# Performance work log

Hardware: AMD Instinct MI355X
Metric: run time of the kernel (lower is better)

Reference implementation:

```python
import jax, jax.numpy as jnp
import numpy as np


def setup_inputs() -> dict:
    key = jax.random.key(0)
    ks = jax.random.split(key, 9)
    bs, nf, h, w = 4, 512, 64, 64
    c8 = nf // 8
    sc = 1.0 / np.sqrt(nf)
    return {
        "x": jax.random.normal(ks[0], (bs, nf, h, w), dtype=jnp.float32),
        "Wq": jax.random.normal(ks[1], (c8, nf), dtype=jnp.float32) * sc,
        "bq": jax.random.normal(ks[2], (c8,), dtype=jnp.float32) * 0.01,
        "Wk": jax.random.normal(ks[3], (c8, nf), dtype=jnp.float32) * sc,
        "bk": jax.random.normal(ks[4], (c8,), dtype=jnp.float32) * 0.01,
        "Wv": jax.random.normal(ks[5], (nf, nf), dtype=jnp.float32) * sc,
        "bv": jax.random.normal(ks[6], (nf,), dtype=jnp.float32) * 0.01,
        "alpha": jax.random.normal(ks[7], (1,), dtype=jnp.float32) * 0.1,
    }


def reference(x, Wq, bq, Wk, bk, Wv, bv, alpha):
    bs, nf, h, w = x.shape
    hw = h * w
    xf = x.reshape(bs, nf, hw)  # flatten spatial; 1x1 conv == channel matmul
    q = jnp.einsum('oc,bcn->bon', Wq, xf) + bq[:, None]  # (bs, c8, hw)
    k = jnp.einsum('oc,bcn->bon', Wk, xf) + bk[:, None]  # (bs, c8, hw)
    v = jnp.einsum('oc,bcn->bon', Wv, xf) + bv[:, None]  # (bs, nf, hw)
    # scores[b, i, j] = key_i . query_j ; softmax over j (queries)
    scores = jnp.einsum('bci,bcj->bij', k, q)  # (bs, hw, hw)
    attn = jax.nn.softmax(scores, axis=-1)
    # out[b, c, i] = sum_j v[b, c, j] * attn[b, i, j]
    out = jnp.einsum('bcj,bij->bci', v, attn).reshape(bs, nf, h, w)
    return x + alpha * out
```

## Files before the change

kernel.cpp:

```cpp
#include <hip/hip_runtime.h>

#define BS 4
#define NF 512
#define HW 4096
#define C8 64
#define TI 32

typedef unsigned short bfu;
typedef __attribute__((ext_vector_type(8))) short bf16x8;
typedef __attribute__((ext_vector_type(4))) float f32x4;

static __device__ __forceinline__ bfu f2bu(float v) {
    union { unsigned int u; float f; } c; c.f = v;
    unsigned int u = c.u;
    u = u + 0x7FFFu + ((u >> 16) & 1u);
    return (bfu)(u >> 16);
}

static __device__ __forceinline__ void gload16(const void* g, void* l) {
    __builtin_amdgcn_global_load_lds(
        (const __attribute__((address_space(1))) unsigned int*)g,
        (__attribute__((address_space(3))) unsigned int*)l,
        16, 0, 0);
}

__global__ __launch_bounds__(256) void k0_xt(const float* __restrict__ x, bfu* __restrict__ xt)
{
    __shared__ float T[64][68];
    const int t  = threadIdx.x;
    const int n0 = blockIdx.x * 64;
    const int c0 = blockIdx.y * 64;
    const int b  = blockIdx.z;

    #pragma unroll
    for (int u = 0; u < 4; u++) {
        int f4 = u * 256 + t;
        int cc = f4 >> 4;
        int n4 = (f4 & 15) << 2;
        float4 v = *(const float4*)(x + ((size_t)(b * NF + c0 + cc)) * HW + n0 + n4);
        *(float4*)&T[cc][n4] = v;
    }
    __syncthreads();
    #pragma unroll
    for (int u = 0; u < 2; u++) {
        int e8 = u * 256 + t;
        int nn = e8 >> 3;
        int c8 = (e8 & 7) << 3;
        union { int4 i4; bfu h[8]; } pk;
        #pragma unroll
        for (int q = 0; q < 8; q++) pk.h[q] = f2bu(T[c8 + q][nn]);
        *(int4*)(xt + ((size_t)(b * HW + n0 + nn)) * NF + c0 + c8) = pk.i4;
    }
}

__global__ __launch_bounds__(256) void k0_w(const float* __restrict__ Wq, const float* __restrict__ bq,
                                            const float* __restrict__ Wk, const float* __restrict__ bk,
                                            const float* __restrict__ Wv, const float* __restrict__ bv,
                                            bfu* __restrict__ Wb, float* __restrict__ bcat)
{
    const int o = blockIdx.x;
    const int t = threadIdx.x;
    const float* src; float bias;
    if (o < 64)       { src = Wq + (size_t)o * NF;          bias = bq[o]; }
    else if (o < 128) { src = Wk + (size_t)(o - 64) * NF;   bias = bk[o - 64]; }
    else              { src = Wv + (size_t)(o - 128) * NF;  bias = bv[o - 128]; }
    float2 v = *(const float2*)(src + t * 2);
    Wb[(size_t)o * NF + t * 2 + 0] = f2bu(v.x);
    Wb[(size_t)o * NF + t * 2 + 1] = f2bu(v.y);
    if (t == 0) bcat[o] = bias;
}

__global__ __launch_bounds__(256) void k1_proj(const bfu* __restrict__ Wb, const float* __restrict__ bcat,
                                               const bfu* __restrict__ xt,
                                               bfu* __restrict__ Qb, bfu* __restrict__ Kb, bfu* __restrict__ Vb)
{
    __shared__ bfu As[128 * 64];
    __shared__ bfu Bs[128 * 64];
    const int t  = threadIdx.x;
    const int o0 = blockIdx.x * 128;
    const int n0 = blockIdx.y * 128;
    const int b  = blockIdx.z;
    const int lane = t & 63, wv = t >> 6;
    const int wm = wv & 1, wn = wv >> 1;
    const int l15 = lane & 15, quad = lane >> 4;

    const int srow = t >> 3;
    const int scol = (t & 7) * 8;

    const bfu* gA = Wb + ((size_t)(o0 + srow)) * NF + scol;
    const bfu* gB = xt + ((size_t)(b * HW + n0 + srow)) * NF + scol;
    bfu* lA = As + t * 8;
    bfu* lB = Bs + t * 8;

    f32x4 acc[4][4];
    #pragma unroll
    for (int m = 0; m < 4; m++)
        #pragma unroll
        for (int n = 0; n < 4; n++) acc[m][n] = (f32x4){0.f, 0.f, 0.f, 0.f};

    for (int c0 = 0; c0 < NF; c0 += 64) {
        __syncthreads();
        #pragma unroll
        for (int p = 0; p < 4; p++) {
            gload16(gA + (size_t)(p * 32) * NF + c0, lA + p * 2048);
            gload16(gB + (size_t)(p * 32) * NF + c0, lB + p * 2048);
        }
        __syncthreads();

        #pragma unroll
        for (int kk = 0; kk < 64; kk += 32) {
            bf16x8 Af[4], Bf[4];
            #pragma unroll
            for (int m = 0; m < 4; m++)
                Af[m] = *(const bf16x8*)(As + (wm * 64 + m * 16 + l15) * 64 + kk + quad * 8);
            #pragma unroll
            for (int n = 0; n < 4; n++)
                Bf[n] = *(const bf16x8*)(Bs + (wn * 64 + n * 16 + l15) * 64 + kk + quad * 8);
            #pragma unroll
            for (int m = 0; m < 4; m++)
                #pragma unroll
                for (int n = 0; n < 4; n++)
                    acc[m][n] = __builtin_amdgcn_mfma_f32_16x16x32_bf16(Af[m], Bf[n], acc[m][n], 0, 0, 0);
        }
    }

    #pragma unroll
    for (int mt = 0; mt < 4; mt++)
        #pragma unroll
        for (int nt = 0; nt < 4; nt++)
            #pragma unroll
            for (int r = 0; r < 4; r++) {
                int go = o0 + wm * 64 + mt * 16 + quad * 4 + r;
                int n  = n0 + wn * 64 + nt * 16 + l15;
                float val = acc[mt][nt][r] + bcat[go];
                if (go < 64)
                    Qb[((size_t)(b * HW + n)) * C8 + go] = f2bu(val);
                else if (go < 128)
                    Kb[((size_t)(b * HW + n)) * C8 + (go - 64)] = f2bu(val);
                else
                    Vb[((size_t)(b * NF + (go - 128))) * HW + n] = f2bu(val);
            }
}

__global__ __launch_bounds__(512, 4) void k23_fused(const bfu* __restrict__ Kb, const bfu* __restrict__ Qb,
                                                    const bfu* __restrict__ Vb,
                                                    const float* __restrict__ x, const float* __restrict__ alpha,
                                                    float* __restrict__ out)
{
    __shared__ bfu   Vs[512 * 64];
    __shared__ bfu   Ps[TI * 72];
    __shared__ float LSum[8][16];
    __shared__ float Scale[TI];

    const int t = threadIdx.x;
    const int lane = t & 63, w = t >> 6;
    const int l15 = lane & 15, quad = lane >> 4;
    const int iq = w >> 2, jq = w & 3;
    const int cw = w * 64;
    const int i0 = blockIdx.x * TI;
    const int b  = blockIdx.y;

    const bfu* kp = Kb + ((size_t)(b * HW + i0 + iq * 16 + l15)) * C8 + quad * 8;
    const bf16x8 Kf0 = *(const bf16x8*)kp;
    const bf16x8 Kf1 = *(const bf16x8*)(kp + 32);

    const bfu* gV = Vb + ((size_t)(b * NF + (t >> 3))) * HW + (t & 7) * 8;
    bfu* lV = Vs + t * 8;

    const bfu* qbase = Qb + ((size_t)(b * HW + jq * 16 + l15)) * C8 + quad * 8;

    f32x4 acc[4][2];
    #pragma unroll
    for (int mt = 0; mt < 4; mt++)
        #pragma unroll
        for (int nt = 0; nt < 2; nt++) acc[mt][nt] = (f32x4){0.f, 0.f, 0.f, 0.f};
    float rsum = 0.f;

    for (int q = 0; q < HW / 64; q++) {
        const int jb = q * 64;
        #pragma unroll
        for (int p = 0; p < 8; p++)
            gload16(gV + (size_t)(p * 64) * HW + jb, lV + p * 4096);

        const bfu* qp = qbase + (size_t)jb * C8;
        bf16x8 A0 = *(const bf16x8*)qp;
        bf16x8 A1 = *(const bf16x8*)(qp + 32);
        f32x4 s = (f32x4){0.f, 0.f, 0.f, 0.f};
        s = __builtin_amdgcn_mfma_f32_16x16x32_bf16(A0, Kf0, s, 0, 0, 0);
        s = __builtin_amdgcn_mfma_f32_16x16x32_bf16(A1, Kf1, s, 0, 0, 0);
        float e0 = __expf(s[0]);
        float e1 = __expf(s[1]);
        float e2 = __expf(s[2]);
        float e3 = __expf(s[3]);
        rsum += (e0 + e1) + (e2 + e3);
        uint2 pk;
        pk.x = (unsigned int)f2bu(e0) | ((unsigned int)f2bu(e1) << 16);
        pk.y = (unsigned int)f2bu(e2) | ((unsigned int)f2bu(e3) << 16);
        *(uint2*)(Ps + (iq * 16 + l15) * 72 + jq * 16 + quad * 4) = pk;

        __syncthreads();

        bf16x8 Pf[2][2];
        #pragma unroll
        for (int nt = 0; nt < 2; nt++)
            #pragma unroll
            for (int kk = 0; kk < 2; kk++)
                Pf[nt][kk] = *(const bf16x8*)(Ps + (nt * 16 + l15) * 72 + kk * 32 + quad * 8);
        #pragma unroll
        for (int mt = 0; mt < 4; mt++) {
            const bfu* vp = Vs + (cw + mt * 16 + l15) * 64 + quad * 8;
            bf16x8 V0 = *(const bf16x8*)vp;
            bf16x8 V1 = *(const bf16x8*)(vp + 32);
            #pragma unroll
            for (int nt = 0; nt < 2; nt++) {
                acc[mt][nt] = __builtin_amdgcn_mfma_f32_16x16x32_bf16(V0, Pf[nt][0], acc[mt][nt], 0, 0, 0);
                acc[mt][nt] = __builtin_amdgcn_mfma_f32_16x16x32_bf16(V1, Pf[nt][1], acc[mt][nt], 0, 0, 0);
            }
        }
        __syncthreads();
    }

    float sred = rsum;
    sred += __shfl_xor(sred, 16, 64);
    sred += __shfl_xor(sred, 32, 64);
    if (quad == 0) LSum[w][l15] = sred;
    __syncthreads();
    if (t < TI) {
        int iqq = t >> 4, il = t & 15;
        float L = (LSum[iqq * 4 + 0][il] + LSum[iqq * 4 + 1][il])
                + (LSum[iqq * 4 + 2][il] + LSum[iqq * 4 + 3][il]);
        Scale[t] = alpha[0] / L;
    }
    __syncthreads();

    #pragma unroll
    for (int nt = 0; nt < 2; nt++) {
        float sc = Scale[nt * 16 + l15];
        int i = i0 + nt * 16 + l15;
        #pragma unroll
        for (int mt = 0; mt < 4; mt++)
            #pragma unroll
            for (int r = 0; r < 4; r++) {
                int c = cw + mt * 16 + quad * 4 + r;
                size_t idx = ((size_t)(b * NF + c)) * HW + i;
                out[idx] = x[idx] + sc * acc[mt][nt][r];
            }
    }
}

extern "C" void kernel_launch(void* const* d_in, const int* in_sizes, int n_in,
                              void* d_out, int out_size, void* d_ws, size_t ws_size,
                              hipStream_t stream)
{
    const float* x     = (const float*)d_in[0];
    const float* Wq    = (const float*)d_in[1];
    const float* bq    = (const float*)d_in[2];
    const float* Wk    = (const float*)d_in[3];
    const float* bk    = (const float*)d_in[4];
    const float* Wv    = (const float*)d_in[5];
    const float* bv    = (const float*)d_in[6];
    const float* alpha = (const float*)d_in[7];
    float* out = (float*)d_out;

    char* ws = (char*)d_ws;
    bfu*   xt   = (bfu*)(ws);
    bfu*   Wb   = (bfu*)(ws + (16u << 20));
    float* bcat = (float*)(ws + (17u << 20));
    bfu*   Qb   = (bfu*)(ws + (18u << 20));
    bfu*   Kb   = (bfu*)(ws + (20u << 20));
    bfu*   Vb   = (bfu*)(ws + (22u << 20));

    k0_xt<<<dim3(HW / 64, NF / 64, BS), 256, 0, stream>>>(x, xt);
    k0_w<<<dim3(640), 256, 0, stream>>>(Wq, bq, Wk, bk, Wv, bv, Wb, bcat);
    k1_proj<<<dim3(5, HW / 128, BS), 256, 0, stream>>>(Wb, bcat, xt, Qb, Kb, Vb);
    k23_fused<<<dim3(HW / TI, BS), 512, 0, stream>>>(Kb, Qb, Vb, x, alpha, out);
}
```

Measured before the change: 272.3 us.

## Load V fragments directly to registers, double-buffer P, remap blocks per XCD

Result: slower. 421.2 us (+54.6%).

```diff
diff --git a/kernel.cpp b/kernel.cpp
--- a/kernel.cpp
+++ b/kernel.cpp
@@ -147,8 +147,7 @@
                                                     const float* __restrict__ x, const float* __restrict__ alpha,
                                                     float* __restrict__ out)
 {
-    __shared__ bfu   Vs[512 * 64];
-    __shared__ bfu   Ps[TI * 72];
+    __shared__ bfu   Ps[2][TI * 72];
     __shared__ float LSum[8][16];
     __shared__ float Scale[TI];
 
@@ -157,17 +156,20 @@
     const int l15 = lane & 15, quad = lane >> 4;
     const int iq = w >> 2, jq = w & 3;
     const int cw = w * 64;
-    const int i0 = blockIdx.x * TI;
-    const int b  = blockIdx.y;
+
+    const int d    = blockIdx.x;
+    const int xcd  = d & 7;
+    const int slot = d >> 3;
+    const int b    = xcd >> 1;
+    const int i0   = ((xcd & 1) * 64 + slot) * TI;
 
     const bfu* kp = Kb + ((size_t)(b * HW + i0 + iq * 16 + l15)) * C8 + quad * 8;
     const bf16x8 Kf0 = *(const bf16x8*)kp;
     const bf16x8 Kf1 = *(const bf16x8*)(kp + 32);
 
-    const bfu* gV = Vb + ((size_t)(b * NF + (t >> 3))) * HW + (t & 7) * 8;
-    bfu* lV = Vs + t * 8;
-
     const bfu* qbase = Qb + ((size_t)(b * HW + jq * 16 + l15)) * C8 + quad * 8;
+
+    const bfu* vbase = Vb + ((size_t)(b * NF + cw + l15)) * HW + quad * 8;
 
     f32x4 acc[4][2];
     #pragma unroll
@@ -178,9 +180,15 @@
 
     for (int q = 0; q < HW / 64; q++) {
         const int jb = q * 64;
-        #pragma unroll
-        for (int p = 0; p < 8; p++)
-            gload16(gV + (size_t)(p * 64) * HW + jb, lV + p * 4096);
+        bfu* Pq = Ps[q & 1];
+
+        bf16x8 Vf0[4], Vf1[4];
+        #pragma unroll
+        for (int mt = 0; mt < 4; mt++) {
+            const bfu* vp = vbase + (size_t)(mt * 16) * HW + jb;
+            Vf0[mt] = *(const bf16x8*)vp;
+            Vf1[mt] = *(const bf16x8*)(vp + 32);
+        }
 
         const bfu* qp = qbase + (size_t)jb * C8;
         bf16x8 A0 = *(const bf16x8*)qp;
@@ -196,7 +204,7 @@
         uint2 pk;
         pk.x = (unsigned int)f2bu(e0) | ((unsigned int)f2bu(e1) << 16);
         pk.y = (unsigned int)f2bu(e2) | ((unsigned int)f2bu(e3) << 16);
-        *(uint2*)(Ps + (iq * 16 + l15) * 72 + jq * 16 + quad * 4) = pk;
+        *(uint2*)(Pq + (iq * 16 + l15) * 72 + jq * 16 + quad * 4) = pk;
 
         __syncthreads();
 
@@ -205,19 +213,15 @@
         for (int nt = 0; nt < 2; nt++)
             #pragma unroll
             for (int kk = 0; kk < 2; kk++)
-                Pf[nt][kk] = *(const bf16x8*)(Ps + (nt * 16 + l15) * 72 + kk * 32 + quad * 8);
+                Pf[nt][kk] = *(const bf16x8*)(Pq + (nt * 16 + l15) * 72 + kk * 32 + quad * 8);
         #pragma unroll
         for (int mt = 0; mt < 4; mt++) {
-            const bfu* vp = Vs + (cw + mt * 16 + l15) * 64 + quad * 8;
-            bf16x8 V0 = *(const bf16x8*)vp;
-            bf16x8 V1 = *(const bf16x8*)(vp + 32);
             #pragma unroll
             for (int nt = 0; nt < 2; nt++) {
-                acc[mt][nt] = __builtin_amdgcn_mfma_f32_16x16x32_bf16(V0, Pf[nt][0], acc[mt][nt], 0, 0, 0);
-                acc[mt][nt] = __builtin_amdgcn_mfma_f32_16x16x32_bf16(V1, Pf[nt][1], acc[mt][nt], 0, 0, 0);
+                acc[mt][nt] = __builtin_amdgcn_mfma_f32_16x16x32_bf16(Vf0[mt], Pf[nt][0], acc[mt][nt], 0, 0, 0);
+                acc[mt][nt] = __builtin_amdgcn_mfma_f32_16x16x32_bf16(Vf1[mt], Pf[nt][1], acc[mt][nt], 0, 0, 0);
             }
         }
-        __syncthreads();
     }
 
     float sred = rsum;
@@ -273,5 +277,5 @@
     k0_xt<<<dim3(HW / 64, NF / 64, BS), 256, 0, stream>>>(x, xt);
     k0_w<<<dim3(640), 256, 0, stream>>>(Wq, bq, Wk, bk, Wv, bv, Wb, bcat);
     k1_proj<<<dim3(5, HW / 128, BS), 256, 0, stream>>>(Wb, bcat, xt, Qb, Kb, Vb);
-    k23_fused<<<dim3(HW / TI, BS), 512, 0, stream>>>(Kb, Qb, Vb, x, alpha, out);
-}
+    k23_fused<<<dim3((HW / TI) * BS), 512, 0, stream>>>(Kb, Qb, Vb, x, alpha, out);
+}
```
